# Kernel tuning notes

Measured on AMD Instinct MI355X. Metric: run time of the kernel, lower is better.

The kernel has to match this reference:

```python
import jax, jax.numpy as jnp
import numpy as np

N_NODES = 50000   # rows of x / output of NF-spmm
M_NODES = 50000   # output of FN-spmm
N_EDGES = 800000
NFEAT, N_HIDDEN, NCLASS = 300, 256, 20
N_IDX = 5000


def setup_inputs() -> dict:
    key = jax.random.key(0)
    ks = jax.random.split(key, 12)
    x = jax.random.normal(ks[0], (N_NODES, NFEAT), dtype=jnp.float32)
    fn_rows = jax.random.randint(ks[1], (N_EDGES,), 0, M_NODES)
    fn_cols = jax.random.randint(ks[2], (N_EDGES,), 0, N_NODES)
    fn_vals = jax.random.uniform(ks[3], (N_EDGES,), dtype=jnp.float32)
    nf_rows = jax.random.randint(ks[4], (N_EDGES,), 0, N_NODES)
    nf_cols = jax.random.randint(ks[5], (N_EDGES,), 0, M_NODES)
    nf_vals = jax.random.uniform(ks[6], (N_EDGES,), dtype=jnp.float32)
    idx = jax.random.randint(ks[7], (N_IDX,), 0, N_NODES)
    # learned parameters (pygcn-style GraphConvolution: spmm(adj, x @ W) + b)
    W1 = jax.random.normal(ks[8], (NFEAT, N_HIDDEN), dtype=jnp.float32) / np.sqrt(NFEAT)
    b1 = jnp.zeros((N_HIDDEN,), dtype=jnp.float32)
    W2 = jax.random.normal(ks[9], (N_HIDDEN, NCLASS), dtype=jnp.float32) / np.sqrt(N_HIDDEN)
    b2 = jnp.zeros((NCLASS,), dtype=jnp.float32)
    return {"x": x, "fn_rows": fn_rows, "fn_cols": fn_cols, "fn_vals": fn_vals,
            "nf_rows": nf_rows, "nf_cols": nf_cols, "nf_vals": nf_vals,
            "idx": idx, "W1": W1, "b1": b1, "W2": W2, "b2": b2}


def _spmm(rows, cols, vals, dense, n_out):
    # sparse(COO) @ dense: gather source rows, scale by edge value, scatter-add.
    return jax.ops.segment_sum(vals[:, None] * dense[cols], rows, num_segments=n_out)


def reference(x, fn_rows, fn_cols, fn_vals, nf_rows, nf_cols, nf_vals, idx, W1, b1, W2, b2):
    # gc1: FN @ (x @ W1) + b1, then relu  (dropout is identity in eval mode)
    h = jax.nn.relu(_spmm(fn_rows, fn_cols, fn_vals, x @ W1, M_NODES) + b1)
    # gc2: NF @ (h @ W2) + b2
    logits = _spmm(nf_rows, nf_cols, nf_vals, h @ W2, N_NODES) + b2
    return jax.nn.softmax(logits, axis=1)[idx]
```

## Files before the change

### kernel.cpp

```cpp
#include <hip/hip_runtime.h>

#define N_NODES 50000
#define M_NODES 50000
#define N_EDGES 800000
#define NFEAT   300
#define NHID    256
#define NCLASS  20
#define N_IDX   5000
#define KTILES  10
#define NTOT    (M_NODES + N_NODES)

typedef __attribute__((ext_vector_type(8))) short bf16x8;
typedef __attribute__((ext_vector_type(4))) float f32x4;

__device__ inline unsigned short f2bf(float f) {
    unsigned u = __float_as_uint(f);
    u += 0x7fff + ((u >> 16) & 1);
    return (unsigned short)(u >> 16);
}
__device__ inline float bf2f(unsigned short h) { return __uint_as_float((unsigned)h << 16); }
__device__ inline float bflo(unsigned v) { return __uint_as_float(v << 16); }
__device__ inline float bfhi(unsigned v) { return __uint_as_float(v & 0xffff0000u); }

__global__ __launch_bounds__(256) void prep_w1_kernel(const float* __restrict__ W1,
                                                      unsigned short* __restrict__ w1h,
                                                      unsigned short* __restrict__ w1l) {
    int id = blockIdx.x * 256 + threadIdx.x;
    if (id >= 320 * 256) return;
    int col = id & 255;
    int k   = id >> 8;
    float v = (k < NFEAT) ? W1[(size_t)k * NHID + col] : 0.f;
    unsigned short hi = f2bf(v);
    unsigned short lo = f2bf(v - bf2f(hi));
    size_t off = (size_t)(k >> 5) * (256 * 32) + (size_t)col * 32 + (k & 31);
    w1h[off] = hi;
    w1l[off] = lo;
}

__global__ __launch_bounds__(256) void gemm1_mfma_kernel(const float* __restrict__ x,
                                                         const unsigned short* __restrict__ w1h,
                                                         const unsigned short* __restrict__ w1l,
                                                         unsigned short* __restrict__ xwb) {
    __shared__ unsigned short Ah[2][64 * 40];
    __shared__ unsigned short Al[2][64 * 40];

    const int tid  = threadIdx.x;
    const int lane = tid & 63;
    const int wv   = tid >> 6;
    const int l15  = lane & 15;
    const int g    = lane >> 4;
    const int row0 = blockIdx.x * 64;

    const int sr = tid >> 2;
    const int sc = tid & 3;
    const bool rowok = (row0 + sr) < N_NODES;
    const float* __restrict__ xrow = x + (size_t)(row0 + sr) * NFEAT;

    float cur[8], nxt[8];
    if (rowok) {
        float4 v0 = *(const float4*)&xrow[sc * 8 + 0];
        float4 v1 = *(const float4*)&xrow[sc * 8 + 4];
        cur[0] = v0.x; cur[1] = v0.y; cur[2] = v0.z; cur[3] = v0.w;
        cur[4] = v1.x; cur[5] = v1.y; cur[6] = v1.z; cur[7] = v1.w;
    } else {
#pragma unroll
        for (int j = 0; j < 8; ++j) cur[j] = 0.f;
    }

    f32x4 acc[4][4];
#pragma unroll
    for (int mf = 0; mf < 4; ++mf)
#pragma unroll
        for (int nf = 0; nf < 4; ++nf) acc[mf][nf] = (f32x4){0.f, 0.f, 0.f, 0.f};

    for (int t = 0; t < KTILES; ++t) {
        if (t < KTILES - 1) {
            const int k0 = (t + 1) * 32 + sc * 8;
            if (t + 1 < KTILES - 1) {
                if (rowok) {
                    float4 v0 = *(const float4*)&xrow[k0 + 0];
                    float4 v1 = *(const float4*)&xrow[k0 + 4];
                    nxt[0] = v0.x; nxt[1] = v0.y; nxt[2] = v0.z; nxt[3] = v0.w;
                    nxt[4] = v1.x; nxt[5] = v1.y; nxt[6] = v1.z; nxt[7] = v1.w;
                } else {
#pragma unroll
                    for (int j = 0; j < 8; ++j) nxt[j] = 0.f;
                }
            } else {
#pragma unroll
                for (int j = 0; j < 8; ++j) {
                    int k = k0 + j;
                    nxt[j] = (rowok && k < NFEAT) ? xrow[k] : 0.f;
                }
            }
        }

        {
            bf16x8 hv, lv;
#pragma unroll
            for (int j = 0; j < 8; ++j) {
                unsigned short h = f2bf(cur[j]);
                hv[j] = (short)h;
                lv[j] = (short)f2bf(cur[j] - bf2f(h));
            }
            const int wo = sr * 40 + sc * 8;
            *(bf16x8*)&Ah[t & 1][wo] = hv;
            *(bf16x8*)&Al[t & 1][wo] = lv;
        }
        __syncthreads();

        const int b = t & 1;
        bf16x8 ah[4], al[4];
#pragma unroll
        for (int mf = 0; mf < 4; ++mf) {
            const int ao = (mf * 16 + l15) * 40 + g * 8;
            ah[mf] = *(const bf16x8*)&Ah[b][ao];
            al[mf] = *(const bf16x8*)&Al[b][ao];
        }
        bf16x8 bh[4], bl[4];
#pragma unroll
        for (int nf = 0; nf < 4; ++nf) {
            const size_t bo = (size_t)t * 8192 + (size_t)(wv * 64 + nf * 16 + l15) * 32 + g * 8;
            bh[nf] = *(const bf16x8*)&w1h[bo];
            bl[nf] = *(const bf16x8*)&w1l[bo];
        }
#pragma unroll
        for (int mf = 0; mf < 4; ++mf)
#pragma unroll
            for (int nf = 0; nf < 4; ++nf) {
                acc[mf][nf] = __builtin_amdgcn_mfma_f32_16x16x32_bf16(ah[mf], bh[nf], acc[mf][nf], 0, 0, 0);
                acc[mf][nf] = __builtin_amdgcn_mfma_f32_16x16x32_bf16(ah[mf], bl[nf], acc[mf][nf], 0, 0, 0);
                acc[mf][nf] = __builtin_amdgcn_mfma_f32_16x16x32_bf16(al[mf], bh[nf], acc[mf][nf], 0, 0, 0);
            }
#pragma unroll
        for (int j = 0; j < 8; ++j) cur[j] = nxt[j];
    }

    const int colb = wv * 64;
#pragma unroll
    for (int mf = 0; mf < 4; ++mf) {
        const int rg0 = row0 + mf * 16 + g * 4;
#pragma unroll
        for (int nf = 0; nf < 4; ++nf) {
            const int cg = colb + nf * 16 + l15;
#pragma unroll
            for (int j = 0; j < 4; ++j) {
                const int rg = rg0 + j;
                if (rg < N_NODES) xwb[(size_t)rg * NHID + cg] = f2bf(acc[mf][nf][j]);
            }
        }
    }
}

__global__ void mark_kernel(const int* __restrict__ idx, int* __restrict__ mark) {
    int i = blockIdx.x * 256 + threadIdx.x;
    if (i < N_IDX) mark[idx[i]] = 1;
}

__global__ __launch_bounds__(256) void hist_both_kernel(const int* __restrict__ fn_rows,
                                                        const int* __restrict__ nf_rows,
                                                        const int* __restrict__ mark,
                                                        int* __restrict__ counts,
                                                        unsigned short* __restrict__ fn_rank,
                                                        unsigned short* __restrict__ nf_rank) {
    const int base = blockIdx.x * 1024 + threadIdx.x;
    int r[4], r2[4], m2[4];
#pragma unroll
    for (int k = 0; k < 4; ++k) {
        int e = base + k * 256;
        r[k]  = (e < N_EDGES) ? fn_rows[e] : -1;
        r2[k] = (e < N_EDGES) ? nf_rows[e] : -1;
    }
#pragma unroll
    for (int k = 0; k < 4; ++k) m2[k] = (r2[k] >= 0) ? mark[r2[k]] : 0;
#pragma unroll
    for (int k = 0; k < 4; ++k) {
        if (r[k] >= 0) {
            int p = atomicAdd(&counts[r[k]], 1);
            fn_rank[base + k * 256] = (unsigned short)p;
        }
    }
#pragma unroll
    for (int k = 0; k < 4; ++k) {
        if (m2[k]) {
            int p = atomicAdd(&counts[M_NODES + r2[k]], 1);
            nf_rank[base + k * 256] = (unsigned short)p;
        }
    }
}

__global__ __launch_bounds__(256) void scan_chunk_kernel(const int* __restrict__ counts,
                                                         int* __restrict__ chunk_incl,
                                                         int* __restrict__ chunk_sums, int n) {
    __shared__ int lds[256];
    int i = blockIdx.x * 256 + threadIdx.x;
    int v = (i < n) ? counts[i] : 0;
    lds[threadIdx.x] = v;
    __syncthreads();
    for (int off = 1; off < 256; off <<= 1) {
        int t = (threadIdx.x >= off) ? lds[threadIdx.x - off] : 0;
        __syncthreads();
        lds[threadIdx.x] += t;
        __syncthreads();
    }
    if (i < n) chunk_incl[i] = lds[threadIdx.x];
    if (threadIdx.x == 255) chunk_sums[blockIdx.x] = lds[255];
}

__global__ __launch_bounds__(512) void scan_sums_kernel(const int* __restrict__ chunk_sums,
                                                        int* __restrict__ chunk_off,
                                                        int* __restrict__ row_ptr_end, int nchunks) {
    __shared__ int lds[512];
    int tid = threadIdx.x;
    int v = (tid < nchunks) ? chunk_sums[tid] : 0;
    lds[tid] = v;
    __syncthreads();
    for (int off = 1; off < 512; off <<= 1) {
        int t = (tid >= off) ? lds[tid - off] : 0;
        __syncthreads();
        lds[tid] += t;
        __syncthreads();
    }
    if (tid < nchunks) chunk_off[tid] = lds[tid] - v;
    if (tid == nchunks - 1) *row_ptr_end = lds[tid];
}

__global__ void scan_apply_kernel(const int* __restrict__ counts,
                                  const int* __restrict__ chunk_incl,
                                  const int* __restrict__ chunk_off,
                                  int* __restrict__ row_ptr, int n) {
    int i = blockIdx.x * 256 + threadIdx.x;
    if (i < n) row_ptr[i] = chunk_incl[i] - counts[i] + chunk_off[blockIdx.x];
}

__global__ __launch_bounds__(256) void scatter_both_kernel(const int* __restrict__ fn_rows,
                                                           const int* __restrict__ fn_cols,
                                                           const float* __restrict__ fn_vals,
                                                           const int* __restrict__ nf_rows,
                                                           const int* __restrict__ nf_cols,
                                                           const float* __restrict__ nf_vals,
                                                           const int* __restrict__ mark,
                                                           const int* __restrict__ row_ptr,
                                                           const unsigned short* __restrict__ fn_rank,
                                                           const unsigned short* __restrict__ nf_rank,
                                                           uint2* __restrict__ csr_cv) {
    const int base = blockIdx.x * 1024 + threadIdx.x;
#pragma unroll
    for (int k = 0; k < 4; ++k) {
        int e = base + k * 256;
        if (e < N_EDGES) {
            int r = fn_rows[e];
            int p = row_ptr[r] + fn_rank[e];
            csr_cv[p] = make_uint2((unsigned)fn_cols[e], __float_as_uint(fn_vals[e]));
        }
    }
#pragma unroll
    for (int k = 0; k < 4; ++k) {
        int e = base + k * 256;
        if (e < N_EDGES) {
            int r2 = nf_rows[e];
            if (mark[r2]) {
                int p = row_ptr[M_NODES + r2] + nf_rank[e];
                csr_cv[p] = make_uint2((unsigned)nf_cols[e], __float_as_uint(nf_vals[e]));
            }
        }
    }
}

__global__ __launch_bounds__(128) void spmm_fn_kernel(const int* __restrict__ row_ptr,
                                                      const uint2* __restrict__ csr_cv,
                                                      const unsigned* __restrict__ xwb,
                                                      const float* __restrict__ b1,
                                                      unsigned* __restrict__ hb) {
    const int r = blockIdx.x;
    const int t = threadIdx.x;
    const int s = row_ptr[r], e = row_ptr[r + 1];
    float a0 = 0.f, a1 = 0.f;
    int j = s;
    for (; j + 3 < e; j += 4) {
        uint2 cv0 = csr_cv[j],     cv1 = csr_cv[j + 1];
        uint2 cv2 = csr_cv[j + 2], cv3 = csr_cv[j + 3];
        float v0 = __uint_as_float(cv0.y), v1 = __uint_as_float(cv1.y);
        float v2 = __uint_as_float(cv2.y), v3 = __uint_as_float(cv3.y);
        unsigned x0 = xwb[(size_t)cv0.x * 128 + t];
        unsigned x1 = xwb[(size_t)cv1.x * 128 + t];
        unsigned x2 = xwb[(size_t)cv2.x * 128 + t];
        unsigned x3 = xwb[(size_t)cv3.x * 128 + t];
        a0 += v0 * bflo(x0); a1 += v0 * bfhi(x0);
        a0 += v1 * bflo(x1); a1 += v1 * bfhi(x1);
        a0 += v2 * bflo(x2); a1 += v2 * bfhi(x2);
        a0 += v3 * bflo(x3); a1 += v3 * bfhi(x3);
    }
    for (; j < e; ++j) {
        uint2 cv = csr_cv[j];
        float v = __uint_as_float(cv.y);
        unsigned xv = xwb[(size_t)cv.x * 128 + t];
        a0 += v * bflo(xv); a1 += v * bfhi(xv);
    }
    float2 bv = *(const float2*)&b1[t * 2];
    float o0 = fmaxf(a0 + bv.x, 0.f);
    float o1 = fmaxf(a1 + bv.y, 0.f);
    hb[(size_t)r * 128 + t] = ((unsigned)f2bf(o1) << 16) | (unsigned)f2bf(o0);
}

__global__ __launch_bounds__(256) void gemm2_kernel(const uint4* __restrict__ hb,
                                                    const float* __restrict__ W2,
                                                    float* __restrict__ hw) {
    __shared__ float w2s[NHID * NCLASS];
    for (int i = threadIdx.x; i < NHID * NCLASS; i += 256) w2s[i] = W2[i];
    __syncthreads();
    int gid = blockIdx.x * 256 + threadIdx.x;
    if (gid >= N_NODES * NCLASS) return;
    int row = gid / NCLASS;
    int col = gid - row * NCLASS;
    const uint4* hp = &hb[(size_t)row * 32];
    float acc = 0.f;
#pragma unroll 4
    for (int k8 = 0; k8 < 32; ++k8) {
        uint4 hv = hp[k8];
        int k = k8 * 8;
        acc += bflo(hv.x) * w2s[(k + 0) * NCLASS + col];
        acc += bfhi(hv.x) * w2s[(k + 1) * NCLASS + col];
        acc += bflo(hv.y) * w2s[(k + 2) * NCLASS + col];
        acc += bfhi(hv.y) * w2s[(k + 3) * NCLASS + col];
        acc += bflo(hv.z) * w2s[(k + 4) * NCLASS + col];
        acc += bfhi(hv.z) * w2s[(k + 5) * NCLASS + col];
        acc += bflo(hv.w) * w2s[(k + 6) * NCLASS + col];
        acc += bfhi(hv.w) * w2s[(k + 7) * NCLASS + col];
    }
    hw[gid] = acc;
}

__global__ __launch_bounds__(64) void spmm_nf_softmax_kernel(const int* __restrict__ idx,
                                                             const int* __restrict__ row_ptr,
                                                             const uint2* __restrict__ csr_cv,
                                                             const float* __restrict__ hw,
                                                             const float* __restrict__ b2,
                                                             float* __restrict__ out) {
    const int b    = blockIdx.x;
    const int lane = threadIdx.x;
    const int r = idx[b];
    const int s = row_ptr[M_NODES + r], e = row_ptr[M_NODES + r + 1];

    float acc[NCLASS];
#pragma unroll
    for (int k = 0; k < NCLASS; ++k) acc[k] = 0.f;

    for (int j = s + lane; j < e; j += 64) {
        uint2 cv = csr_cv[j];
        int   c = (int)cv.x;
        float v = __uint_as_float(cv.y);
        const float4* hp = (const float4*)&hw[(size_t)c * NCLASS];
        float4 h0 = hp[0], h1 = hp[1], h2 = hp[2], h3 = hp[3], h4 = hp[4];
        acc[0]  += v * h0.x; acc[1]  += v * h0.y; acc[2]  += v * h0.z; acc[3]  += v * h0.w;
        acc[4]  += v * h1.x; acc[5]  += v * h1.y; acc[6]  += v * h1.z; acc[7]  += v * h1.w;
        acc[8]  += v * h2.x; acc[9]  += v * h2.y; acc[10] += v * h2.z; acc[11] += v * h2.w;
        acc[12] += v * h3.x; acc[13] += v * h3.y; acc[14] += v * h3.z; acc[15] += v * h3.w;
        acc[16] += v * h4.x; acc[17] += v * h4.y; acc[18] += v * h4.z; acc[19] += v * h4.w;
    }

#pragma unroll
    for (int k = 0; k < NCLASS; ++k) {
#pragma unroll
        for (int off = 1; off < 64; off <<= 1) acc[k] += __shfl_xor(acc[k], off, 64);
    }

    if (lane == 0) {
        float v[NCLASS];
        float m = -1e30f;
#pragma unroll
        for (int k = 0; k < NCLASS; ++k) {
            v[k] = acc[k] + b2[k];
            m = fmaxf(m, v[k]);
        }
        float sum = 0.f;
#pragma unroll
        for (int k = 0; k < NCLASS; ++k) {
            v[k] = __expf(v[k] - m);
            sum += v[k];
        }
        float inv = 1.f / sum;
#pragma unroll
        for (int k = 0; k < NCLASS; ++k) out[(size_t)b * NCLASS + k] = v[k] * inv;
    }
}

extern "C" void kernel_launch(void* const* d_in, const int* in_sizes, int n_in,
                              void* d_out, int out_size, void* d_ws, size_t ws_size,
                              hipStream_t stream) {
    const float* x       = (const float*)d_in[0];
    const int*   fn_rows = (const int*)  d_in[1];
    const int*   fn_cols = (const int*)  d_in[2];
    const float* fn_vals = (const float*)d_in[3];
    const int*   nf_rows = (const int*)  d_in[4];
    const int*   nf_cols = (const int*)  d_in[5];
    const float* nf_vals = (const float*)d_in[6];
    const int*   idx     = (const int*)  d_in[7];
    const float* W1      = (const float*)d_in[8];
    const float* b1      = (const float*)d_in[9];
    const float* W2      = (const float*)d_in[10];
    const float* b2      = (const float*)d_in[11];
    float* out = (float*)d_out;

    size_t off = 0;
    auto alloc = [&](size_t bytes) {
        void* p = (char*)d_ws + off;
        off += (bytes + 255) & ~(size_t)255;
        return p;
    };
    unsigned short* xwb = (unsigned short*)alloc((size_t)N_NODES * NHID * 2);
    unsigned*       hb  = (unsigned*)      alloc((size_t)M_NODES * NHID * 2);
    float* hw       = (float*)alloc((size_t)M_NODES * NCLASS * 4);
    int*   counts   = (int*)  alloc((size_t)NTOT * 4);
    int*   mark     = (int*)  alloc((size_t)N_NODES * 4);
    int*   row_ptr  = (int*)  alloc((size_t)(NTOT + 1) * 4);
    uint2* csr_cv   = (uint2*)alloc((size_t)2 * N_EDGES * 8);
    unsigned short* fn_rank = (unsigned short*)alloc((size_t)N_EDGES * 2);
    unsigned short* nf_rank = (unsigned short*)alloc((size_t)N_EDGES * 2);
    int*   chunk_incl = (int*)alloc((size_t)NTOT * 4);
    int*   chunk_sums = (int*)alloc(512 * 4);
    int*   chunk_off  = (int*)alloc(512 * 4);
    unsigned short* w1h = (unsigned short*)alloc((size_t)KTILES * 256 * 32 * 2);
    unsigned short* w1l = (unsigned short*)alloc((size_t)KTILES * 256 * 32 * 2);
    (void)ws_size; (void)n_in; (void)in_sizes; (void)out_size;

    const int NCHUNKS_ALL = (NTOT + 255) / 256;
    const int EB4 = (N_EDGES + 1023) / 1024;

    size_t zlen = (size_t)((char*)mark - (char*)counts) + (size_t)N_NODES * 4;
    hipMemsetAsync(counts, 0, zlen, stream);

    mark_kernel<<<(N_IDX + 255) / 256, 256, 0, stream>>>(idx, mark);

    prep_w1_kernel<<<320, 256, 0, stream>>>(W1, w1h, w1l);
    gemm1_mfma_kernel<<<(N_NODES + 63) / 64, 256, 0, stream>>>(x, w1h, w1l, xwb);

    hist_both_kernel<<<EB4, 256, 0, stream>>>(fn_rows, nf_rows, mark, counts, fn_rank, nf_rank);
    scan_chunk_kernel<<<NCHUNKS_ALL, 256, 0, stream>>>(counts, chunk_incl, chunk_sums, NTOT);
    scan_sums_kernel<<<1, 512, 0, stream>>>(chunk_sums, chunk_off, &row_ptr[NTOT], NCHUNKS_ALL);
    scan_apply_kernel<<<NCHUNKS_ALL, 256, 0, stream>>>(counts, chunk_incl, chunk_off, row_ptr, NTOT);
    scatter_both_kernel<<<EB4, 256, 0, stream>>>(fn_rows, fn_cols, fn_vals,
                                                 nf_rows, nf_cols, nf_vals,
                                                 mark, row_ptr, fn_rank, nf_rank, csr_cv);

    spmm_fn_kernel<<<M_NODES, 128, 0, stream>>>(row_ptr, csr_cv, (const unsigned*)xwb, b1, hb);

    gemm2_kernel<<<(N_NODES * NCLASS + 255) / 256, 256, 0, stream>>>((const uint4*)hb, W2, hw);

    spmm_nf_softmax_kernel<<<N_IDX, 64, 0, stream>>>(idx, row_ptr, csr_cv, hw, b2, out);
}
```

Before: 220.8 us.

## Split FN spmm rows into column slices with edge-parallel lanes and shuffle reduction

Replaces the one-block-per-row FN spmm (128 threads, each owning two hidden columns) with eight 64-thread blocks per row. Each block covers a 16-column slice, and the four 16-lane groups handle different edges in parallel, combined at the end by cross-lane shuffle reductions. The aim is more memory-level parallelism and more in-flight gathers per row for rows with few edges (around 16 on average). In exchange, each gather is only 64 bytes wide, the CSR entries are re-read by all eight slice blocks, and the launch has 400k small blocks. The grid is sized with N_NODES where the output has M_NODES rows; the two are equal here.

```diff
diff --git a/kernel.cpp b/kernel.cpp
--- a/kernel.cpp
+++ b/kernel.cpp
@@ -267,40 +267,48 @@
     }
 }
 
-__global__ __launch_bounds__(128) void spmm_fn_kernel(const int* __restrict__ row_ptr,
-                                                      const uint2* __restrict__ csr_cv,
-                                                      const unsigned* __restrict__ xwb,
-                                                      const float* __restrict__ b1,
-                                                      unsigned* __restrict__ hb) {
-    const int r = blockIdx.x;
-    const int t = threadIdx.x;
+__global__ __launch_bounds__(64) void spmm_fn_sliced_kernel(const int* __restrict__ row_ptr,
+                                                            const uint2* __restrict__ csr_cv,
+                                                            const unsigned* __restrict__ xwb,
+                                                            const float* __restrict__ b1,
+                                                            unsigned* __restrict__ hb) {
+    const int bid  = blockIdx.x;
+    const int r    = bid >> 3;
+    const int p    = bid & 7;
+    const int lane = threadIdx.x;
+    const int nl   = lane & 15;
+    const int eo   = lane >> 4;
     const int s = row_ptr[r], e = row_ptr[r + 1];
+    const unsigned* __restrict__ xslice = xwb + p * 16 + nl;
+
     float a0 = 0.f, a1 = 0.f;
-    int j = s;
-    for (; j + 3 < e; j += 4) {
-        uint2 cv0 = csr_cv[j],     cv1 = csr_cv[j + 1];
-        uint2 cv2 = csr_cv[j + 2], cv3 = csr_cv[j + 3];
-        float v0 = __uint_as_float(cv0.y), v1 = __uint_as_float(cv1.y);
-        float v2 = __uint_as_float(cv2.y), v3 = __uint_as_float(cv3.y);
-        unsigned x0 = xwb[(size_t)cv0.x * 128 + t];
-        unsigned x1 = xwb[(size_t)cv1.x * 128 + t];
-        unsigned x2 = xwb[(size_t)cv2.x * 128 + t];
-        unsigned x3 = xwb[(size_t)cv3.x * 128 + t];
-        a0 += v0 * bflo(x0); a1 += v0 * bfhi(x0);
-        a0 += v1 * bflo(x1); a1 += v1 * bfhi(x1);
-        a0 += v2 * bflo(x2); a1 += v2 * bfhi(x2);
-        a0 += v3 * bflo(x3); a1 += v3 * bfhi(x3);
-    }
-    for (; j < e; ++j) {
-        uint2 cv = csr_cv[j];
-        float v = __uint_as_float(cv.y);
-        unsigned xv = xwb[(size_t)cv.x * 128 + t];
-        a0 += v * bflo(xv); a1 += v * bfhi(xv);
-    }
-    float2 bv = *(const float2*)&b1[t * 2];
-    float o0 = fmaxf(a0 + bv.x, 0.f);
-    float o1 = fmaxf(a1 + bv.y, 0.f);
-    hb[(size_t)r * 128 + t] = ((unsigned)f2bf(o1) << 16) | (unsigned)f2bf(o0);
+    for (int j0 = s; j0 < e; j0 += 8) {
+        const int j1 = j0 + eo, j2 = j0 + 4 + eo;
+        uint2 cv1 = make_uint2(0u, 0u), cv2 = make_uint2(0u, 0u);
+        unsigned xv1 = 0u, xv2 = 0u;
+        if (j1 < e) {
+            cv1 = csr_cv[j1];
+            xv1 = xslice[(size_t)cv1.x * 128];
+        }
+        if (j2 < e) {
+            cv2 = csr_cv[j2];
+            xv2 = xslice[(size_t)cv2.x * 128];
+        }
+        float v1 = __uint_as_float(cv1.y), v2 = __uint_as_float(cv2.y);
+        a0 += v1 * bflo(xv1); a1 += v1 * bfhi(xv1);
+        a0 += v2 * bflo(xv2); a1 += v2 * bfhi(xv2);
+    }
+
+    a0 += __shfl_xor(a0, 16, 64); a1 += __shfl_xor(a1, 16, 64);
+    a0 += __shfl_xor(a0, 32, 64); a1 += __shfl_xor(a1, 32, 64);
+
+    if (eo == 0) {
+        const int col2 = p * 16 + nl;
+        float2 bv = *(const float2*)&b1[col2 * 2];
+        float o0 = fmaxf(a0 + bv.x, 0.f);
+        float o1 = fmaxf(a1 + bv.y, 0.f);
+        hb[(size_t)r * 128 + col2] = ((unsigned)f2bf(o1) << 16) | (unsigned)f2bf(o0);
+    }
 }
 
 __global__ __launch_bounds__(256) void gemm2_kernel(const uint4* __restrict__ hb,
@@ -443,7 +451,8 @@
                                                  nf_rows, nf_cols, nf_vals,
                                                  mark, row_ptr, fn_rank, nf_rank, csr_cv);
 
-    spmm_fn_kernel<<<M_NODES, 128, 0, stream>>>(row_ptr, csr_cv, (const unsigned*)xwb, b1, hb);
+    spmm_fn_sliced_kernel<<<N_NODES * 8, 64, 0, stream>>>(row_ptr, csr_cv,
+                                                          (const unsigned*)xwb, b1, hb);
 
     gemm2_kernel<<<(N_NODES * NCLASS + 255) / 256, 256, 0, stream>>>((const uint4*)hb, W2, hw);
 
```

Result: slower. 321.1 us (+45.4%).
